# Performance work log

Measured on AMD Instinct MI355X. Metric: run time of the kernel, lower is better.

## Reference

```python
import jax, jax.numpy as jnp
import numpy as np
import math

N = 50000
E = 1600000
A = 100          # num_atoms
H = 64           # hidden_dim / node_dim
L = 5            # num_layers
NB = 8           # num_basis
LMAX = 2
CUTOFF = 5.0


def setup_inputs() -> dict:
    key = jax.random.key(0)
    ks = jax.random.split(key, 32)
    s = 0.05
    inp = {
        'atomic_numbers': jax.random.randint(ks[0], (N,), 0, A),
        'pos': jax.random.normal(ks[1], (N, 3), jnp.float32) * 2.0,
        'edge_index': jax.random.randint(ks[2], (2, E), 0, N),
        # GaussianBasis widths
        'widths': jnp.ones((NB,), jnp.float32) * 0.5,
        # node embedding
        'embed': jax.random.normal(ks[3], (A, H), jnp.float32),
        # per-layer params, stacked on leading layer dim
        'rad_w1': jax.random.normal(ks[4], (L, NB, H), jnp.float32) * s,
        'rad_b1': jnp.zeros((L, H), jnp.float32),
        'rad_w2': jax.random.normal(ks[5], (L, H, H * (LMAX + 1)), jnp.float32) * s,
        'rad_b2': jnp.zeros((L, H * (LMAX + 1)), jnp.float32),
        'self_w': jax.random.normal(ks[6], (L, H, H), jnp.float32) * s,
        'self_b': jnp.zeros((L, H), jnp.float32),
        'proj_w': jax.random.normal(ks[7], (L, 2 * H, H), jnp.float32) * s,
        'proj_b': jnp.zeros((L, H), jnp.float32),
        'mlp_w1': jax.random.normal(ks[8], (L, H, 2 * H), jnp.float32) * s,
        'mlp_b1': jnp.zeros((L, 2 * H), jnp.float32),
        'mlp_w2': jax.random.normal(ks[9], (L, 2 * H, H), jnp.float32) * s,
        'mlp_b2': jnp.zeros((L, H), jnp.float32),
        'ln_g': jnp.ones((L, H), jnp.float32),
        'ln_b': jnp.zeros((L, H), jnp.float32),
        # readout MLP
        'ro_w1': jax.random.normal(ks[10], (H, H), jnp.float32) * s,
        'ro_b1': jnp.zeros((H,), jnp.float32),
        'ro_w2': jax.random.normal(ks[11], (H, H // 2), jnp.float32) * s,
        'ro_b2': jnp.zeros((H // 2,), jnp.float32),
        'ro_w3': jax.random.normal(ks[12], (H // 2, 1), jnp.float32) * s,
        'ro_b3': jnp.zeros((1,), jnp.float32),
        # per-species reference energies
        'atomic_e': jax.random.normal(ks[13], (A, 1), jnp.float32) * s,
    }
    return inp


def _layer_norm(x, g, b, eps=1e-5):
    mu = jnp.mean(x, axis=-1, keepdims=True)
    var = jnp.var(x, axis=-1, keepdims=True)
    return (x - mu) * jax.lax.rsqrt(var + eps) * g + b


def _spherical_harmonics(edge_vec):
    # real SH up to lmax=2, [E, 9] (computed for fidelity; unused by conv math)
    r = jnp.clip(jnp.linalg.norm(edge_vec, axis=-1), 1e-8, None)
    x, y, z = edge_vec[:, 0] / r, edge_vec[:, 1] / r, edge_vec[:, 2] / r
    x2, y2, z2 = x * x, y * y, z * z
    return jnp.stack([
        jnp.full_like(x, 0.28209479177387814),
        -0.4886025119029199 * y, 0.4886025119029199 * z, -0.4886025119029199 * x,
        1.0925484305920792 * x * y, -1.0925484305920792 * y * z,
        0.94617469575756 * z2 - 0.31539156525252 * (x2 + y2),
        -1.0925484305920792 * x * z, 0.5462742152960396 * (x2 - y2),
    ], axis=-1)


def _forward(atomic_numbers, pos, edge_index, widths, embed,
             rad_w1, rad_b1, rad_w2, rad_b2, self_w, self_b, proj_w, proj_b,
             mlp_w1, mlp_b1, mlp_w2, mlp_b2, ln_g, ln_b,
             ro_w1, ro_b1, ro_w2, ro_b2, ro_w3, ro_b3, atomic_e):
    n = pos.shape[0]
    row, col = edge_index[0], edge_index[1]
    edge_vec = pos[col] - pos[row]                          # [E,3]
    edge_len = jnp.linalg.norm(edge_vec, axis=-1, keepdims=True)  # [E,1]

    # GaussianBasis
    xr = edge_len / CUTOFF
    cut = 0.5 * (jnp.cos(xr * math.pi) + 1.0)
    cut = cut * (edge_len < CUTOFF).astype(jnp.float32)     # [E,1]
    centers = jnp.linspace(0.0, CUTOFF, NB)
    diff = edge_len - centers                               # [E,NB]
    edge_rbf = jnp.exp(-0.5 * (diff / jnp.clip(widths, 0.1, None)) ** 2) * cut

    edge_sh = _spherical_harmonics(edge_vec)  # computed but unused, as in source

    feats = embed[atomic_numbers]                           # [N,H]
    for i in range(L):
        # radial net -> per-edge weights [E, H*(lmax+1)]
        w = jax.nn.silu(edge_rbf @ rad_w1[i] + rad_b1[i]) @ rad_w2[i] + rad_b2[i]
        # messages: node_j[:,:,None] * w.view(E,H,lmax+1) summed over last dim
        # == node_j * w.reshape(E,H,lmax+1).sum(-1)
        wsum = w.reshape(-1, H, LMAX + 1).sum(axis=-1)      # [E,H]
        messages = feats[col] * wsum                        # gather + multiply
        agg = jax.ops.segment_sum(messages, row, num_segments=n)  # scatter-add
        self_out = feats @ self_w[i] + self_b[i]
        conv_out = jnp.concatenate([self_out, agg], axis=-1) @ proj_w[i] + proj_b[i]
        upd = jax.nn.silu(conv_out @ mlp_w1[i] + mlp_b1[i]) @ mlp_w2[i] + mlp_b2[i]
        feats = _layer_norm(feats + upd, ln_g[i], ln_b[i])

    h = jax.nn.silu(feats @ ro_w1 + ro_b1)
    h = jax.nn.silu(h @ ro_w2 + ro_b2)
    atomic_energies = h @ ro_w3 + ro_b3                     # [N,1]
    atomic_energies = atomic_energies + atomic_e[atomic_numbers]
    return atomic_energies.sum()                            # batch=None path


def reference(atomic_numbers, pos, edge_index, widths, embed,
              rad_w1, rad_b1, rad_w2, rad_b2, self_w, self_b, proj_w, proj_b,
              mlp_w1, mlp_b1, mlp_w2, mlp_b2, ln_g, ln_b,
              ro_w1, ro_b1, ro_w2, ro_b2, ro_w3, ro_b3, atomic_e):
    return _forward(atomic_numbers, pos, edge_index, widths, embed,
                    rad_w1, rad_b1, rad_w2, rad_b2, self_w, self_b, proj_w, proj_b,
                    mlp_w1, mlp_b1, mlp_w2, mlp_b2, ln_g, ln_b,
                    ro_w1, ro_b1, ro_w2, ro_b2, ro_w3, ro_b3, atomic_e)
```

## Files before the change

kernel.cpp:

```cpp
#include <hip/hip_runtime.h>
#include <hip/hip_fp16.h>
#include <math.h>

constexpr int N_NODES = 50000;
constexpr int N_EDGES = 1600000;
constexpr int HDIM    = 64;
constexpr int NLAYER  = 5;
constexpr int NBASIS  = 8;
constexpr int TLUT    = 256;
constexpr float CUT_R = 5.0f;
constexpr float PI_F  = 3.14159265358979f;

constexpr int NBKT = 196;
constexpr int BCAP = 9216;
constexpr int TILE = 2048;

typedef __attribute__((ext_vector_type(8))) short short8;
typedef __attribute__((ext_vector_type(4))) float f32x4;
#define MFMA16 __builtin_amdgcn_mfma_f32_16x16x32_bf16

__device__ __forceinline__ float siluf(float x) { return x / (1.0f + __expf(-x)); }

__device__ __forceinline__ unsigned int f2bf(float x) {
    unsigned int b = __float_as_uint(x);
    return (b + 0x7fffu + ((b >> 16) & 1u)) >> 16;
}
__device__ __forceinline__ float bf_lo(unsigned int u) { return __uint_as_float(u << 16); }
__device__ __forceinline__ float bf_hi(unsigned int u) { return __uint_as_float(u & 0xffff0000u); }

__device__ __forceinline__ unsigned int f2e5(float x) {
    unsigned short b = __half_as_ushort(__float2half(x));
    return ((unsigned int)b + 0x7Fu + ((b >> 8) & 1u)) >> 8;
}
__device__ __forceinline__ float e5f(unsigned int u8) {
    return __half2float(__ushort_as_half((unsigned short)(u8 << 8)));
}

__device__ __forceinline__ int blockScan256Excl(int cv, int tid, int* wtot) {
    int v = cv;
    int lane = tid & 63;
    #pragma unroll
    for (int off = 1; off < 64; off <<= 1) {
        int t = __shfl_up(v, off, 64);
        if (lane >= off) v += t;
    }
    if (lane == 63) wtot[tid >> 6] = v;
    __syncthreads();
    int pre = 0;
    #pragma unroll
    for (int w = 0; w < 4; ++w)
        if (w < (tid >> 6)) pre += wtot[w];
    __syncthreads();
    return v + pre - cv;
}


__global__ void k_embed(const int* __restrict__ an, const float* __restrict__ embed,
                        unsigned short* __restrict__ featsbf,
                        unsigned char* __restrict__ featsf8) {
    int i = blockIdx.x * blockDim.x + threadIdx.x;
    if (i >= N_NODES * HDIM) return;
    int node = i >> 6, h = i & 63;
    float v = embed[an[node] * HDIM + h];
    featsbf[i] = (unsigned short)f2bf(v);
    featsf8[i] = (unsigned char)f2e5(v);
}

__global__ void k_edge(const int* __restrict__ row, const int* __restrict__ col,
                       const float* __restrict__ pos,
                       unsigned int* __restrict__ rec4, unsigned char* __restrict__ bkt) {
    int e = blockIdx.x * blockDim.x + threadIdx.x;
    if (e >= N_EDGES) return;
    int r = row[e], c = col[e];
    float dx = pos[c * 3 + 0] - pos[r * 3 + 0];
    float dy = pos[c * 3 + 1] - pos[r * 3 + 1];
    float dz = pos[c * 3 + 2] - pos[r * 3 + 2];
    float len = sqrtf(dx * dx + dy * dy + dz * dz);
    float t = len * ((float)(TLUT - 1) / CUT_R);
    t = fminf(t, (float)(TLUT - 1));
    unsigned int nn = (unsigned int)(t + 0.5f);
    if (nn > TLUT - 1) nn = TLUT - 1;
    rec4[e] = ((unsigned int)c << 16) | (nn << 8) | ((unsigned int)r & 255u);
    bkt[e]  = (unsigned char)(r >> 8);
}

__global__ __launch_bounds__(256) void k_binA(const unsigned int* __restrict__ rec4,
                                              const unsigned char* __restrict__ bkt,
                                              int* __restrict__ btail,
                                              unsigned int* __restrict__ binned) {
    __shared__ unsigned int ent[TILE];
    __shared__ short bb[TILE];
    __shared__ unsigned int sorted[TILE];
    __shared__ short sortedB[TILE];
    __shared__ int cnt[256], cnt2[256], base[256], gbase[256];
    __shared__ int wtot[4];
    const int tid = threadIdx.x;
    const int t0  = blockIdx.x * TILE;
    const int nv  = min(TILE, N_EDGES - t0);

    cnt[tid] = 0;
    __syncthreads();

    #pragma unroll
    for (int i = 0; i < TILE / 256; ++i) {
        int idx = i * 256 + tid;
        if (idx < nv) {
            ent[idx] = rec4[t0 + idx];
            int b = bkt[t0 + idx];
            bb[idx] = (short)b;
            atomicAdd(&cnt[b], 1);
        }
    }
    __syncthreads();
    int cv = cnt[tid];
    int excl = blockScan256Excl(cv, tid, wtot);
    base[tid] = excl;
    if (tid < NBKT && cv > 0) gbase[tid] = atomicAdd(&btail[tid], cv);
    cnt2[tid] = excl;
    __syncthreads();
    #pragma unroll
    for (int i = 0; i < TILE / 256; ++i) {
        int idx = i * 256 + tid;
        if (idx < nv) {
            int b = bb[idx];
            int p = atomicAdd(&cnt2[b], 1);
            sorted[p]  = ent[idx];
            sortedB[p] = (short)b;
        }
    }
    __syncthreads();
    for (int s = tid; s < nv; s += 256) {
        int b = sortedB[s];
        binned[(size_t)b * BCAP + gbase[b] + (s - base[b])] = sorted[s];
    }
}

__global__ void k_scanB(const int* __restrict__ btail, int* __restrict__ bbase) {
    __shared__ int wtot[4];
    int t = threadIdx.x;
    int v = (t < NBKT) ? btail[t] : 0;
    int excl = blockScan256Excl(v, t, wtot);
    if (t < NBKT) bbase[t] = excl;
}

__global__ __launch_bounds__(256) void k_binB(const unsigned int* __restrict__ binned,
                                              const int* __restrict__ btail,
                                              const int* __restrict__ bbase,
                                              int* __restrict__ starts,
                                              unsigned int* __restrict__ erec) {
    __shared__ int hist[256];
    __shared__ int cur[256];
    __shared__ int wtot[4];
    const int b = blockIdx.x;
    const int node0 = b << 8;
    const int t = threadIdx.x;
    hist[t] = 0;
    __syncthreads();
    const int cnt = btail[b];
    const unsigned int* src = binned + (size_t)b * BCAP;
    for (int s = t; s < cnt; s += 256)
        atomicAdd(&hist[src[s] & 255u], 1);
    __syncthreads();
    int h = hist[t];
    int excl = bbase[b] + blockScan256Excl(h, t, wtot);
    int n = node0 + t;
    if (n < N_NODES) starts[n] = excl;
    if (b == 0 && t == 0) starts[N_NODES] = N_EDGES;
    cur[t] = excl;
    __syncthreads();
    for (int s = t; s < cnt; s += 256) {
        unsigned int p = src[s];
        int pp = atomicAdd(&cur[p & 255u], 1);
        erec[pp] = p;
    }
}

__global__ void k_prep(const float* __restrict__ rad_w2, const float* __restrict__ self_w,
                       const float* __restrict__ proj_w,
                       const float* __restrict__ rad_b2, const float* __restrict__ self_b,
                       const float* __restrict__ proj_b,
                       float* __restrict__ W2s, float* __restrict__ Wsp,
                       float* __restrict__ b2s, float* __restrict__ bsp) {
    int i = blockIdx.x * blockDim.x + threadIdx.x;
    if (i < NLAYER * HDIM * HDIM) {
        int l = i / (HDIM * HDIM); int rem = i % (HDIM * HDIM);
        int k = rem / HDIM; int h = rem % HDIM;
        const float* w = rad_w2 + ((size_t)l * HDIM + k) * (HDIM * 3) + h * 3;
        W2s[i] = w[0] + w[1] + w[2];
        const float* sw = self_w + ((size_t)l * HDIM + k) * HDIM;
        const float* pw = proj_w + (size_t)l * 2 * HDIM * HDIM;
        float acc = 0.f;
        for (int m = 0; m < HDIM; ++m) acc += sw[m] * pw[m * HDIM + h];
        Wsp[i] = acc;
    } else {
        int i2 = i - NLAYER * HDIM * HDIM;
        if (i2 >= NLAYER * HDIM) return;
        int l = i2 / HDIM, h = i2 % HDIM;
        const float* rb2 = rad_b2 + l * HDIM * 3 + h * 3;
        b2s[i2] = rb2[0] + rb2[1] + rb2[2];
        float acc = proj_b[l * HDIM + h];
        const float* pw = proj_w + (size_t)l * 2 * HDIM * HDIM;
        const float* sb = self_b + l * HDIM;
        for (int m = 0; m < HDIM; ++m) acc += sb[m] * pw[m * HDIM + h];
        bsp[i2] = acc;
    }
}

__global__ void k_wtr(const float* __restrict__ Wsp, const float* __restrict__ proj_w,
                      const float* __restrict__ mlp_w1, const float* __restrict__ mlp_w2,
                      const float* __restrict__ ro_w1, const float* __restrict__ ro_w2,
                      unsigned short* __restrict__ WspT, unsigned short* __restrict__ PbT,
                      unsigned short* __restrict__ W1T, unsigned short* __restrict__ W2T,
                      unsigned short* __restrict__ Ro1T, unsigned short* __restrict__ Ro2T) {
    int i = blockIdx.x * blockDim.x + threadIdx.x;
    if (i < NLAYER * 24576) {
        int l = i / 24576, off = i % 24576;
        if (off < 4096) {
            int n = off >> 6, k = off & 63;
            WspT[(size_t)l * 4096 + off] = (unsigned short)f2bf(Wsp[(size_t)l * 4096 + k * 64 + n]);
        } else if (off < 8192) {
            int o = off - 4096; int n = o >> 6, k = o & 63;
            PbT[(size_t)l * 4096 + o] =
                (unsigned short)f2bf(proj_w[(size_t)l * 8192 + (64 + k) * 64 + n]);
        } else if (off < 16384) {
            int o = off - 8192; int n = o >> 6, k = o & 63;
            W1T[(size_t)l * 8192 + o] = (unsigned short)f2bf(mlp_w1[(size_t)l * 8192 + k * 128 + n]);
        } else {
            int o = off - 16384; int n = o >> 7, k = o & 127;
            W2T[(size_t)l * 8192 + o] = (unsigned short)f2bf(mlp_w2[(size_t)l * 8192 + k * 64 + n]);
        }
    } else {
        int i2 = i - NLAYER * 24576;
        if (i2 >= 6144) return;
        if (i2 < 4096) {
            int n = i2 >> 6, k = i2 & 63;
            Ro1T[i2] = (unsigned short)f2bf(ro_w1[k * 64 + n]);
        } else {
            int o = i2 - 4096; int n = o >> 6, k = o & 63;
            Ro2T[o] = (unsigned short)f2bf(ro_w2[k * 32 + n]);
        }
    }
}

__global__ void k_lut(const float* __restrict__ widths, const float* __restrict__ rad_w1,
                      const float* __restrict__ rad_b1, const float* __restrict__ W2s,
                      const float* __restrict__ b2s, unsigned short* __restrict__ lutB) {
    int bid = blockIdx.x;
    int l = bid / TLUT, t = bid % TLUT;
    int h = threadIdx.x;
    __shared__ float h1s[HDIM];
    float len = (float)t * (CUT_R / (float)(TLUT - 1));
    float cut = 0.0f;
    if (len < CUT_R) cut = 0.5f * (cosf(len * (PI_F / CUT_R)) + 1.0f);
    float acc = rad_b1[l * HDIM + h];
    for (int b = 0; b < NBASIS; ++b) {
        float wb = fmaxf(widths[b], 0.1f);
        float center = (float)b * (CUT_R / (float)(NBASIS - 1));
        float d = (len - center) / wb;
        float rbf = __expf(-0.5f * d * d) * cut;
        acc += rbf * rad_w1[(l * NBASIS + b) * HDIM + h];
    }
    h1s[h] = siluf(acc);
    __syncthreads();
    float o = b2s[l * HDIM + h];
    const float* w2 = W2s + (size_t)l * HDIM * HDIM;
    for (int k = 0; k < HDIM; ++k) o += h1s[k] * w2[k * HDIM + h];
    lutB[(size_t)bid * HDIM + h] = (unsigned short)f2bf(o);
}


__global__ __launch_bounds__(256) void k_agg(const uint2* __restrict__ featsf8_2,
                                             const uint4* __restrict__ lutB4_l,
                                             const int* __restrict__ starts,
                                             const unsigned int* __restrict__ erec,
                                             uint4* __restrict__ aggbf4) {
    int wid  = (blockIdx.x * blockDim.x + threadIdx.x) >> 6;
    int lane = threadIdx.x & 63;
    int slot = lane >> 3;
    int j    = lane & 7;
    if (wid >= N_NODES) return;
    int e0 = starts[wid], e1 = starts[wid + 1];
    float a0 = 0, a1 = 0, a2 = 0, a3 = 0, a4 = 0, a5 = 0, a6 = 0, a7 = 0;
    #pragma unroll 2
    for (int e = e0 + slot; e < e1; e += 8) {
        unsigned int rec = erec[e];
        int c  = rec >> 16;
        int i0 = (rec >> 8) & 255;
        uint4 qw = lutB4_l[i0 * 8 + j];
        uint2 fb = featsf8_2[(size_t)c * 8 + j];
        a0 += e5f(fb.x & 255u)         * bf_lo(qw.x);
        a1 += e5f((fb.x >> 8) & 255u)  * bf_hi(qw.x);
        a2 += e5f((fb.x >> 16) & 255u) * bf_lo(qw.y);
        a3 += e5f(fb.x >> 24)          * bf_hi(qw.y);
        a4 += e5f(fb.y & 255u)         * bf_lo(qw.z);
        a5 += e5f((fb.y >> 8) & 255u)  * bf_hi(qw.z);
        a6 += e5f((fb.y >> 16) & 255u) * bf_lo(qw.w);
        a7 += e5f(fb.y >> 24)          * bf_hi(qw.w);
    }
    #pragma unroll
    for (int off = 8; off < 64; off <<= 1) {
        a0 += __shfl_xor(a0, off, 64);  a1 += __shfl_xor(a1, off, 64);
        a2 += __shfl_xor(a2, off, 64);  a3 += __shfl_xor(a3, off, 64);
        a4 += __shfl_xor(a4, off, 64);  a5 += __shfl_xor(a5, off, 64);
        a6 += __shfl_xor(a6, off, 64);  a7 += __shfl_xor(a7, off, 64);
    }
    if (slot == 0) {
        uint4 o;
        o.x = f2bf(a0) | (f2bf(a1) << 16);
        o.y = f2bf(a2) | (f2bf(a3) << 16);
        o.z = f2bf(a4) | (f2bf(a5) << 16);
        o.w = f2bf(a6) | (f2bf(a7) << 16);
        aggbf4[(size_t)wid * 8 + j] = o;
    }
}

constexpr int BP = 72;
__global__ __launch_bounds__(256) void k_node(
        unsigned short* __restrict__ featsbf,
        unsigned char* __restrict__ featsf8,
        const unsigned short* __restrict__ aggbf,
        const unsigned short* __restrict__ WspT_l, const unsigned short* __restrict__ PbT_l,
        const unsigned short* __restrict__ W1T_l, const unsigned short* __restrict__ W2T_l,
        const float* __restrict__ bsp_l,
        const float* __restrict__ mlp_b1_l, const float* __restrict__ mlp_b2_l,
        const float* __restrict__ ln_g_l, const float* __restrict__ ln_b_l) {
    __shared__ unsigned short P[64 * BP];
    __shared__ unsigned short Q[64 * BP];
    __shared__ unsigned short S[64 * BP];
    const int tid  = threadIdx.x;
    const int lane = tid & 63;
    const int wib  = tid >> 6;
    const int mt   = __builtin_amdgcn_readfirstlane(wib);
    const int nb0  = blockIdx.x * 64;
    const int colL = lane & 15;
    const int kgrp = lane >> 4;

    #pragma unroll 4
    for (int i = 0; i < 16; ++i) {
        int r  = wib + i * 4;
        int nd = nb0 + r; nd = (nd < N_NODES) ? nd : (N_NODES - 1);
        P[r * BP + lane] = featsbf[(size_t)nd * 64 + lane];
        Q[r * BP + lane] = aggbf[(size_t)nd * 64 + lane];
    }
    __syncthreads();

    float xres[4][4];
    #pragma unroll
    for (int j = 0; j < 4; ++j)
        #pragma unroll
        for (int nt = 0; nt < 4; ++nt)
            xres[nt][j] = bf_lo(P[(mt * 16 + kgrp * 4 + j) * BP + nt * 16 + colL]);

    f32x4 acc[4];
    #pragma unroll
    for (int nt = 0; nt < 4; ++nt) {
        float b = bsp_l[nt * 16 + colL];
        acc[nt][0] = b; acc[nt][1] = b; acc[nt][2] = b; acc[nt][3] = b;
    }
    #pragma unroll
    for (int kb = 0; kb < 2; ++kb) {
        short8 ax = *(const short8*)&P[(mt * 16 + colL) * BP + kb * 32 + kgrp * 8];
        short8 aa = *(const short8*)&Q[(mt * 16 + colL) * BP + kb * 32 + kgrp * 8];
        #pragma unroll
        for (int nt = 0; nt < 4; ++nt) {
            short8 bw = *(const short8*)&WspT_l[(nt * 16 + colL) * 64 + kb * 32 + kgrp * 8];
            acc[nt] = MFMA16(ax, bw, acc[nt], 0, 0, 0);
            short8 bp = *(const short8*)&PbT_l[(nt * 16 + colL) * 64 + kb * 32 + kgrp * 8];
            acc[nt] = MFMA16(aa, bp, acc[nt], 0, 0, 0);
        }
    }
    __syncthreads();
    #pragma unroll
    for (int nt = 0; nt < 4; ++nt)
        #pragma unroll
        for (int j = 0; j < 4; ++j)
            P[(mt * 16 + kgrp * 4 + j) * BP + nt * 16 + colL] = (unsigned short)f2bf(acc[nt][j]);
    __syncthreads();

    {
        f32x4 m[8];
        #pragma unroll
        for (int nt = 0; nt < 8; ++nt) {
            float b = mlp_b1_l[nt * 16 + colL];
            m[nt][0] = b; m[nt][1] = b; m[nt][2] = b; m[nt][3] = b;
        }
        #pragma unroll
        for (int kb = 0; kb < 2; ++kb) {
            short8 ac = *(const short8*)&P[(mt * 16 + colL) * BP + kb * 32 + kgrp * 8];
            #pragma unroll
            for (int nt = 0; nt < 8; ++nt) {
                short8 bw = *(const short8*)&W1T_l[(nt * 16 + colL) * 64 + kb * 32 + kgrp * 8];
                m[nt] = MFMA16(ac, bw, m[nt], 0, 0, 0);
            }
        }
        __syncthreads();
        #pragma unroll
        for (int nt = 0; nt < 4; ++nt)
            #pragma unroll
            for (int j = 0; j < 4; ++j)
                Q[(mt * 16 + kgrp * 4 + j) * BP + nt * 16 + colL] =
                    (unsigned short)f2bf(siluf(m[nt][j]));
        #pragma unroll
        for (int nt = 4; nt < 8; ++nt)
            #pragma unroll
            for (int j = 0; j < 4; ++j)
                S[(mt * 16 + kgrp * 4 + j) * BP + (nt - 4) * 16 + colL] =
                    (unsigned short)f2bf(siluf(m[nt][j]));
    }
    __syncthreads();

    f32x4 u[4];
    #pragma unroll
    for (int nt = 0; nt < 4; ++nt) {
        float b = mlp_b2_l[nt * 16 + colL];
        u[nt][0] = b; u[nt][1] = b; u[nt][2] = b; u[nt][3] = b;
    }
    #pragma unroll
    for (int kb = 0; kb < 4; ++kb) {
        short8 am = (kb < 2)
            ? *(const short8*)&Q[(mt * 16 + colL) * BP + kb * 32 + kgrp * 8]
            : *(const short8*)&S[(mt * 16 + colL) * BP + (kb - 2) * 32 + kgrp * 8];
        #pragma unroll
        for (int nt = 0; nt < 4; ++nt) {
            short8 bw = *(const short8*)&W2T_l[(nt * 16 + colL) * 128 + kb * 32 + kgrp * 8];
            u[nt] = MFMA16(am, bw, u[nt], 0, 0, 0);
        }
    }

    float y[4][4];
    float s1[4] = {0, 0, 0, 0}, s2[4] = {0, 0, 0, 0};
    #pragma unroll
    for (int j = 0; j < 4; ++j) {
        #pragma unroll
        for (int nt = 0; nt < 4; ++nt) {
            float v = xres[nt][j] + u[nt][j];
            y[nt][j] = v;
            s1[j] += v; s2[j] += v * v;
        }
    }
    #pragma unroll
    for (int off = 1; off < 16; off <<= 1) {
        #pragma unroll
        for (int j = 0; j < 4; ++j) {
            s1[j] += __shfl_xor(s1[j], off, 64);
            s2[j] += __shfl_xor(s2[j], off, 64);
        }
    }
    float gv[4], bv[4];
    #pragma unroll
    for (int nt = 0; nt < 4; ++nt) {
        gv[nt] = ln_g_l[nt * 16 + colL];
        bv[nt] = ln_b_l[nt * 16 + colL];
    }
    #pragma unroll
    for (int j = 0; j < 4; ++j) {
        int node = nb0 + mt * 16 + kgrp * 4 + j;
        if (node >= N_NODES) continue;
        float mu  = s1[j] * (1.0f / 64.0f);
        float var = s2[j] * (1.0f / 64.0f) - mu * mu;
        float rr  = rsqrtf(var + 1e-5f);
        #pragma unroll
        for (int nt = 0; nt < 4; ++nt) {
            float o = (y[nt][j] - mu) * rr * gv[nt] + bv[nt];
            size_t idx = (size_t)node * 64 + nt * 16 + colL;
            featsbf[idx] = (unsigned short)f2bf(o);
            featsf8[idx] = (unsigned char)f2e5(o);
        }
    }
}


__global__ __launch_bounds__(256) void k_readout(const unsigned short* __restrict__ featsbf,
        const int* __restrict__ an,
        const unsigned short* __restrict__ Ro1T, const unsigned short* __restrict__ Ro2T,
        const float* __restrict__ ro_b1, const float* __restrict__ ro_b2,
        const float* __restrict__ ro_w3, const float* __restrict__ ro_b3,
        const float* __restrict__ atomic_e, float* __restrict__ blockpart) {
    __shared__ unsigned short P[64 * BP];
    __shared__ unsigned short Q[64 * BP];
    __shared__ float sred[256];
    const int tid  = threadIdx.x;
    const int lane = tid & 63;
    const int wib  = tid >> 6;
    const int mt   = __builtin_amdgcn_readfirstlane(wib);
    const int nb0  = blockIdx.x * 64;
    const int colL = lane & 15;
    const int kgrp = lane >> 4;

    #pragma unroll 4
    for (int i = 0; i < 16; ++i) {
        int r  = wib + i * 4;
        int nd = nb0 + r; nd = (nd < N_NODES) ? nd : (N_NODES - 1);
        P[r * BP + lane] = featsbf[(size_t)nd * 64 + lane];
    }
    __syncthreads();

    {
        f32x4 m[4];
        #pragma unroll
        for (int nt = 0; nt < 4; ++nt) {
            float b = ro_b1[nt * 16 + colL];
            m[nt][0] = b; m[nt][1] = b; m[nt][2] = b; m[nt][3] = b;
        }
        #pragma unroll
        for (int kb = 0; kb < 2; ++kb) {
            short8 ax = *(const short8*)&P[(mt * 16 + colL) * BP + kb * 32 + kgrp * 8];
            #pragma unroll
            for (int nt = 0; nt < 4; ++nt) {
                short8 bw = *(const short8*)&Ro1T[(nt * 16 + colL) * 64 + kb * 32 + kgrp * 8];
                m[nt] = MFMA16(ax, bw, m[nt], 0, 0, 0);
            }
        }
        __syncthreads();
        #pragma unroll
        for (int nt = 0; nt < 4; ++nt)
            #pragma unroll
            for (int j = 0; j < 4; ++j)
                Q[(mt * 16 + kgrp * 4 + j) * BP + nt * 16 + colL] =
                    (unsigned short)f2bf(siluf(m[nt][j]));
    }
    __syncthreads();

    f32x4 u[2];
    #pragma unroll
    for (int nt = 0; nt < 2; ++nt) {
        float b = ro_b2[nt * 16 + colL];
        u[nt][0] = b; u[nt][1] = b; u[nt][2] = b; u[nt][3] = b;
    }
    #pragma unroll
    for (int kb = 0; kb < 2; ++kb) {
        short8 am = *(const short8*)&Q[(mt * 16 + colL) * BP + kb * 32 + kgrp * 8];
        #pragma unroll
        for (int nt = 0; nt < 2; ++nt) {
            short8 bw = *(const short8*)&Ro2T[(nt * 16 + colL) * 64 + kb * 32 + kgrp * 8];
            u[nt] = MFMA16(am, bw, u[nt], 0, 0, 0);
        }
    }
    float w3[2];
    #pragma unroll
    for (int nt = 0; nt < 2; ++nt) w3[nt] = ro_w3[nt * 16 + colL];
    float part = 0.0f;
    #pragma unroll
    for (int j = 0; j < 4; ++j) {
        float c = siluf(u[0][j]) * w3[0] + siluf(u[1][j]) * w3[1];
        #pragma unroll
        for (int off = 1; off < 16; off <<= 1) c += __shfl_xor(c, off, 64);
        int node = nb0 + mt * 16 + kgrp * 4 + j;
        if (colL == 0 && node < N_NODES)
            part += c + ro_b3[0] + atomic_e[an[node]];
    }
    sred[tid] = part;
    __syncthreads();
    for (int off = 128; off > 0; off >>= 1) {
        if (tid < off) sred[tid] += sred[tid + off];
        __syncthreads();
    }
    if (tid == 0) blockpart[blockIdx.x] = sred[0];
}

__global__ void k_final(const float* __restrict__ blockpart, int nb, float* __restrict__ out) {
    __shared__ float s[256];
    float acc = 0.f;
    for (int i = threadIdx.x; i < nb; i += 256) acc += blockpart[i];
    s[threadIdx.x] = acc; __syncthreads();
    for (int off = 128; off > 0; off >>= 1) {
        if (threadIdx.x < off) s[threadIdx.x] += s[threadIdx.x + off];
        __syncthreads();
    }
    if (threadIdx.x == 0) out[0] = s[0];
}


extern "C" void kernel_launch(void* const* d_in, const int* in_sizes, int n_in,
                              void* d_out, int out_size, void* d_ws, size_t ws_size,
                              hipStream_t stream) {
    const int*   an       = (const int*)  d_in[0];
    const float* pos      = (const float*)d_in[1];
    const int*   edge     = (const int*)  d_in[2];
    const float* widths   = (const float*)d_in[3];
    const float* embed    = (const float*)d_in[4];
    const float* rad_w1   = (const float*)d_in[5];
    const float* rad_b1   = (const float*)d_in[6];
    const float* rad_w2   = (const float*)d_in[7];
    const float* rad_b2   = (const float*)d_in[8];
    const float* self_w   = (const float*)d_in[9];
    const float* self_b   = (const float*)d_in[10];
    const float* proj_w   = (const float*)d_in[11];
    const float* proj_b   = (const float*)d_in[12];
    const float* mlp_w1   = (const float*)d_in[13];
    const float* mlp_b1   = (const float*)d_in[14];
    const float* mlp_w2   = (const float*)d_in[15];
    const float* mlp_b2   = (const float*)d_in[16];
    const float* ln_g     = (const float*)d_in[17];
    const float* ln_b     = (const float*)d_in[18];
    const float* ro_w1    = (const float*)d_in[19];
    const float* ro_b1    = (const float*)d_in[20];
    const float* ro_w2    = (const float*)d_in[21];
    const float* ro_b2    = (const float*)d_in[22];
    const float* ro_w3    = (const float*)d_in[23];
    const float* ro_b3    = (const float*)d_in[24];
    const float* atomic_e = (const float*)d_in[25];

    char* w = (char*)d_ws;
    auto alloc = [&](size_t bytes) { char* p = w; w += (bytes + 255) & ~(size_t)255; return p; };
    unsigned short* featsbf = (unsigned short*)alloc(sizeof(unsigned short) * N_NODES * HDIM);
    unsigned char* featsf8  = (unsigned char*)alloc(sizeof(unsigned char) * N_NODES * HDIM);
    unsigned short* aggbf   = (unsigned short*)alloc(sizeof(unsigned short) * N_NODES * HDIM);
    unsigned short* lutB = (unsigned short*)alloc(sizeof(unsigned short) * NLAYER * TLUT * HDIM);
    float* W2s       = (float*)alloc(sizeof(float) * NLAYER * HDIM * HDIM);
    float* b2s       = (float*)alloc(sizeof(float) * NLAYER * HDIM);
    float* Wsp       = (float*)alloc(sizeof(float) * NLAYER * HDIM * HDIM);
    float* bsp       = (float*)alloc(sizeof(float) * NLAYER * HDIM);
    unsigned short* WspT = (unsigned short*)alloc(sizeof(unsigned short) * NLAYER * 4096);
    unsigned short* PbT  = (unsigned short*)alloc(sizeof(unsigned short) * NLAYER * 4096);
    unsigned short* W1T  = (unsigned short*)alloc(sizeof(unsigned short) * NLAYER * 8192);
    unsigned short* W2T  = (unsigned short*)alloc(sizeof(unsigned short) * NLAYER * 8192);
    unsigned short* Ro1T = (unsigned short*)alloc(sizeof(unsigned short) * 4096);
    unsigned short* Ro2T = (unsigned short*)alloc(sizeof(unsigned short) * 2048);
    unsigned int* erec = (unsigned int*)alloc(sizeof(unsigned int) * N_EDGES);
    unsigned int* rec4 = (unsigned int*)alloc(sizeof(unsigned int) * N_EDGES);
    unsigned char* bkt = (unsigned char*)alloc(sizeof(unsigned char) * N_EDGES);
    unsigned int* binned = (unsigned int*)alloc(sizeof(unsigned int) * (size_t)NBKT * BCAP);
    int*   btail     = (int*)  alloc(sizeof(int) * 256);
    int*   bbase     = (int*)  alloc(sizeof(int) * 256);
    int*   starts    = (int*)  alloc(sizeof(int) * (N_NODES + 1));
    float* blockpart = (float*)alloc(sizeof(float) * 1024);
    (void)ws_size; (void)in_sizes; (void)n_in; (void)out_size;

    const int* erow = edge;
    const int* ecol = edge + N_EDGES;

    hipMemsetAsync(btail, 0, sizeof(int) * 256, stream);
    k_embed<<<12500, 256, 0, stream>>>(an, embed, featsbf, featsf8);
    k_edge<<<(N_EDGES + 255) / 256, 256, 0, stream>>>(erow, ecol, pos, rec4, bkt);
    k_binA<<<(N_EDGES + TILE - 1) / TILE, 256, 0, stream>>>(rec4, bkt, btail, binned);
    k_scanB<<<1, 256, 0, stream>>>(btail, bbase);
    k_binB<<<NBKT, 256, 0, stream>>>(binned, btail, bbase, starts, erec);
    k_prep<<<(NLAYER * HDIM * HDIM + NLAYER * HDIM + 255) / 256, 256, 0, stream>>>(
        rad_w2, self_w, proj_w, rad_b2, self_b, proj_b, W2s, Wsp, b2s, bsp);
    k_wtr<<<(NLAYER * 24576 + 6144 + 255) / 256, 256, 0, stream>>>(
        Wsp, proj_w, mlp_w1, mlp_w2, ro_w1, ro_w2, WspT, PbT, W1T, W2T, Ro1T, Ro2T);
    k_lut<<<NLAYER * TLUT, 64, 0, stream>>>(widths, rad_w1, rad_b1, W2s, b2s, lutB);

    for (int l = 0; l < NLAYER; ++l) {
        k_agg<<<12500, 256, 0, stream>>>((const uint2*)featsf8,
                                         (const uint4*)(lutB + (size_t)l * TLUT * HDIM),
                                         starts, erec, (uint4*)aggbf);
        k_node<<<782, 256, 0, stream>>>(featsbf, featsf8, aggbf,
            WspT + (size_t)l * 4096, PbT + (size_t)l * 4096,
            W1T + (size_t)l * 8192, W2T + (size_t)l * 8192,
            bsp + l * HDIM, mlp_b1 + l * 2 * HDIM, mlp_b2 + l * HDIM,
            ln_g + l * HDIM, ln_b + l * HDIM);
    }

    k_readout<<<782, 256, 0, stream>>>(featsbf, an, Ro1T, Ro2T, ro_b1, ro_b2,
                                       ro_w3, ro_b3, atomic_e, blockpart);
    k_final<<<1, 256, 0, stream>>>(blockpart, 782, (float*)d_out);
}
```

Before: 395.9 us.

## Fuse edge aggregation into per-layer node kernel with ping-pong feature buffers

Merges the aggregation kernel into the node-update kernel. Each wave now gathers neighbor messages for its 16 nodes and writes them straight into shared memory, instead of writing aggregates to global memory and reading them back. Because other blocks still read the previous layer's features, the features are double-buffered, and the readout reads the final buffer. This removes one launch per layer and the aggregate round trip through global memory. In exchange, only 782 blocks of 4 waves do the gather, each wave handling 16 nodes serially, which lowers parallelism and latency hiding for the memory-bound gather compared with 12500 blocks.

```diff
diff --git a/kernel.cpp b/kernel.cpp
--- a/kernel.cpp
+++ b/kernel.cpp
@@ -268,57 +268,12 @@
     lutB[(size_t)bid * HDIM + h] = (unsigned short)f2bf(o);
 }
 
-
-__global__ __launch_bounds__(256) void k_agg(const uint2* __restrict__ featsf8_2,
-                                             const uint4* __restrict__ lutB4_l,
-                                             const int* __restrict__ starts,
-                                             const unsigned int* __restrict__ erec,
-                                             uint4* __restrict__ aggbf4) {
-    int wid  = (blockIdx.x * blockDim.x + threadIdx.x) >> 6;
-    int lane = threadIdx.x & 63;
-    int slot = lane >> 3;
-    int j    = lane & 7;
-    if (wid >= N_NODES) return;
-    int e0 = starts[wid], e1 = starts[wid + 1];
-    float a0 = 0, a1 = 0, a2 = 0, a3 = 0, a4 = 0, a5 = 0, a6 = 0, a7 = 0;
-    #pragma unroll 2
-    for (int e = e0 + slot; e < e1; e += 8) {
-        unsigned int rec = erec[e];
-        int c  = rec >> 16;
-        int i0 = (rec >> 8) & 255;
-        uint4 qw = lutB4_l[i0 * 8 + j];
-        uint2 fb = featsf8_2[(size_t)c * 8 + j];
-        a0 += e5f(fb.x & 255u)         * bf_lo(qw.x);
-        a1 += e5f((fb.x >> 8) & 255u)  * bf_hi(qw.x);
-        a2 += e5f((fb.x >> 16) & 255u) * bf_lo(qw.y);
-        a3 += e5f(fb.x >> 24)          * bf_hi(qw.y);
-        a4 += e5f(fb.y & 255u)         * bf_lo(qw.z);
-        a5 += e5f((fb.y >> 8) & 255u)  * bf_hi(qw.z);
-        a6 += e5f((fb.y >> 16) & 255u) * bf_lo(qw.w);
-        a7 += e5f(fb.y >> 24)          * bf_hi(qw.w);
-    }
-    #pragma unroll
-    for (int off = 8; off < 64; off <<= 1) {
-        a0 += __shfl_xor(a0, off, 64);  a1 += __shfl_xor(a1, off, 64);
-        a2 += __shfl_xor(a2, off, 64);  a3 += __shfl_xor(a3, off, 64);
-        a4 += __shfl_xor(a4, off, 64);  a5 += __shfl_xor(a5, off, 64);
-        a6 += __shfl_xor(a6, off, 64);  a7 += __shfl_xor(a7, off, 64);
-    }
-    if (slot == 0) {
-        uint4 o;
-        o.x = f2bf(a0) | (f2bf(a1) << 16);
-        o.y = f2bf(a2) | (f2bf(a3) << 16);
-        o.z = f2bf(a4) | (f2bf(a5) << 16);
-        o.w = f2bf(a6) | (f2bf(a7) << 16);
-        aggbf4[(size_t)wid * 8 + j] = o;
-    }
-}
-
 constexpr int BP = 72;
-__global__ __launch_bounds__(256) void k_node(
-        unsigned short* __restrict__ featsbf,
-        unsigned char* __restrict__ featsf8,
-        const unsigned short* __restrict__ aggbf,
+__global__ __launch_bounds__(256) void k_layer(
+        const unsigned short* __restrict__ fbR, const unsigned char* __restrict__ f8R,
+        unsigned short* __restrict__ fbW, unsigned char* __restrict__ f8W,
+        const uint4* __restrict__ lutB4_l,
+        const int* __restrict__ starts, const unsigned int* __restrict__ erec,
         const unsigned short* __restrict__ WspT_l, const unsigned short* __restrict__ PbT_l,
         const unsigned short* __restrict__ W1T_l, const unsigned short* __restrict__ W2T_l,
         const float* __restrict__ bsp_l,
@@ -334,13 +289,55 @@
     const int nb0  = blockIdx.x * 64;
     const int colL = lane & 15;
     const int kgrp = lane >> 4;
+    const uint2* f8R2 = (const uint2*)f8R;
 
     #pragma unroll 4
     for (int i = 0; i < 16; ++i) {
         int r  = wib + i * 4;
         int nd = nb0 + r; nd = (nd < N_NODES) ? nd : (N_NODES - 1);
-        P[r * BP + lane] = featsbf[(size_t)nd * 64 + lane];
-        Q[r * BP + lane] = aggbf[(size_t)nd * 64 + lane];
+        P[r * BP + lane] = fbR[(size_t)nd * 64 + lane];
+    }
+
+    {
+        int slot = lane >> 3, j = lane & 7;
+        for (int i = 0; i < 16; ++i) {
+            int r  = mt * 16 + i;
+            int nd = nb0 + r;
+            if (nd >= N_NODES) break;
+            int e0 = starts[nd], e1 = starts[nd + 1];
+            float a0 = 0, a1 = 0, a2 = 0, a3 = 0, a4 = 0, a5 = 0, a6 = 0, a7 = 0;
+            #pragma unroll 2
+            for (int e = e0 + slot; e < e1; e += 8) {
+                unsigned int rec = erec[e];
+                int c  = rec >> 16;
+                int i0 = (rec >> 8) & 255;
+                uint4 qw = lutB4_l[i0 * 8 + j];
+                uint2 fb = f8R2[(size_t)c * 8 + j];
+                a0 += e5f(fb.x & 255u)         * bf_lo(qw.x);
+                a1 += e5f((fb.x >> 8) & 255u)  * bf_hi(qw.x);
+                a2 += e5f((fb.x >> 16) & 255u) * bf_lo(qw.y);
+                a3 += e5f(fb.x >> 24)          * bf_hi(qw.y);
+                a4 += e5f(fb.y & 255u)         * bf_lo(qw.z);
+                a5 += e5f((fb.y >> 8) & 255u)  * bf_hi(qw.z);
+                a6 += e5f((fb.y >> 16) & 255u) * bf_lo(qw.w);
+                a7 += e5f(fb.y >> 24)          * bf_hi(qw.w);
+            }
+            #pragma unroll
+            for (int off = 8; off < 64; off <<= 1) {
+                a0 += __shfl_xor(a0, off, 64);  a1 += __shfl_xor(a1, off, 64);
+                a2 += __shfl_xor(a2, off, 64);  a3 += __shfl_xor(a3, off, 64);
+                a4 += __shfl_xor(a4, off, 64);  a5 += __shfl_xor(a5, off, 64);
+                a6 += __shfl_xor(a6, off, 64);  a7 += __shfl_xor(a7, off, 64);
+            }
+            if (slot == 0) {
+                uint4 o;
+                o.x = f2bf(a0) | (f2bf(a1) << 16);
+                o.y = f2bf(a2) | (f2bf(a3) << 16);
+                o.z = f2bf(a4) | (f2bf(a5) << 16);
+                o.w = f2bf(a6) | (f2bf(a7) << 16);
+                *(uint4*)&Q[r * BP + 8 * j] = o;
+            }
+        }
     }
     __syncthreads();
 
@@ -463,8 +460,8 @@
         for (int nt = 0; nt < 4; ++nt) {
             float o = (y[nt][j] - mu) * rr * gv[nt] + bv[nt];
             size_t idx = (size_t)node * 64 + nt * 16 + colL;
-            featsbf[idx] = (unsigned short)f2bf(o);
-            featsf8[idx] = (unsigned char)f2e5(o);
+            fbW[idx] = (unsigned short)f2bf(o);
+            f8W[idx] = (unsigned char)f2e5(o);
         }
     }
 }
@@ -603,9 +600,10 @@
 
     char* w = (char*)d_ws;
     auto alloc = [&](size_t bytes) { char* p = w; w += (bytes + 255) & ~(size_t)255; return p; };
-    unsigned short* featsbf = (unsigned short*)alloc(sizeof(unsigned short) * N_NODES * HDIM);
-    unsigned char* featsf8  = (unsigned char*)alloc(sizeof(unsigned char) * N_NODES * HDIM);
-    unsigned short* aggbf   = (unsigned short*)alloc(sizeof(unsigned short) * N_NODES * HDIM);
+    unsigned short* featsbf0 = (unsigned short*)alloc(sizeof(unsigned short) * N_NODES * HDIM);
+    unsigned short* featsbf1 = (unsigned short*)alloc(sizeof(unsigned short) * N_NODES * HDIM);
+    unsigned char* featsf80  = (unsigned char*)alloc(sizeof(unsigned char) * N_NODES * HDIM);
+    unsigned char* featsf81  = (unsigned char*)alloc(sizeof(unsigned char) * N_NODES * HDIM);
     unsigned short* lutB = (unsigned short*)alloc(sizeof(unsigned short) * NLAYER * TLUT * HDIM);
     float* W2s       = (float*)alloc(sizeof(float) * NLAYER * HDIM * HDIM);
     float* b2s       = (float*)alloc(sizeof(float) * NLAYER * HDIM);
@@ -631,7 +629,7 @@
     const int* ecol = edge + N_EDGES;
 
     hipMemsetAsync(btail, 0, sizeof(int) * 256, stream);
-    k_embed<<<12500, 256, 0, stream>>>(an, embed, featsbf, featsf8);
+    k_embed<<<12500, 256, 0, stream>>>(an, embed, featsbf0, featsf80);
     k_edge<<<(N_EDGES + 255) / 256, 256, 0, stream>>>(erow, ecol, pos, rec4, bkt);
     k_binA<<<(N_EDGES + TILE - 1) / TILE, 256, 0, stream>>>(rec4, bkt, btail, binned);
     k_scanB<<<1, 256, 0, stream>>>(btail, bbase);
@@ -643,17 +641,19 @@
     k_lut<<<NLAYER * TLUT, 64, 0, stream>>>(widths, rad_w1, rad_b1, W2s, b2s, lutB);
 
     for (int l = 0; l < NLAYER; ++l) {
-        k_agg<<<12500, 256, 0, stream>>>((const uint2*)featsf8,
-                                         (const uint4*)(lutB + (size_t)l * TLUT * HDIM),
-                                         starts, erec, (uint4*)aggbf);
-        k_node<<<782, 256, 0, stream>>>(featsbf, featsf8, aggbf,
+        const unsigned short* fbR = (l & 1) ? featsbf1 : featsbf0;
+        const unsigned char*  f8R = (l & 1) ? featsf81 : featsf80;
+        unsigned short*       fbW = (l & 1) ? featsbf0 : featsbf1;
+        unsigned char*        f8W = (l & 1) ? featsf80 : featsf81;
+        k_layer<<<782, 256, 0, stream>>>(fbR, f8R, fbW, f8W,
+            (const uint4*)(lutB + (size_t)l * TLUT * HDIM), starts, erec,
             WspT + (size_t)l * 4096, PbT + (size_t)l * 4096,
             W1T + (size_t)l * 8192, W2T + (size_t)l * 8192,
             bsp + l * HDIM, mlp_b1 + l * 2 * HDIM, mlp_b2 + l * HDIM,
             ln_g + l * HDIM, ln_b + l * HDIM);
     }
 
-    k_readout<<<782, 256, 0, stream>>>(featsbf, an, Ro1T, Ro2T, ro_b1, ro_b2,
+    k_readout<<<782, 256, 0, stream>>>(featsbf1, an, Ro1T, Ro2T, ro_b1, ro_b2,
                                        ro_w3, ro_b3, atomic_e, blockpart);
     k_final<<<1, 256, 0, stream>>>(blockpart, 782, (float*)d_out);
 }
```

Result: slower. 450.2 us (+13.7%).
